# Kernel tuning notes

Measured on AMD Instinct MI355X. Metric: run time of the kernel, lower is better.

Reference implementation:

```python
import jax, jax.numpy as jnp
import numpy as np

B, M, IN, H, D = 64, 512, 256, 4, 64
N = B * M
E = N * 16


def setup_inputs() -> dict:
    key = jax.random.key(0)
    ks = jax.random.split(key, 12)
    s = 1.0 / np.sqrt(IN)
    return {
        "query_input": jax.random.normal(ks[0], (N, IN), jnp.float32),
        "source_input": jax.random.normal(ks[1], (N, IN), jnp.float32),
        "edge_weight": jax.random.uniform(ks[2], (E,), jnp.float32),
        "Wq_w": jax.random.normal(ks[3], (IN, H * D), jnp.float32) * s,
        "Wq_b": jax.random.normal(ks[4], (H * D,), jnp.float32) * s,
        "Wk_w": jax.random.normal(ks[5], (IN, H * D), jnp.float32) * s,
        "Wk_b": jax.random.normal(ks[6], (H * D,), jnp.float32) * s,
        "Wv_w": jax.random.normal(ks[7], (IN, H * D), jnp.float32) * s,
        "Wv_b": jax.random.normal(ks[8], (H * D,), jnp.float32) * s,
        "n_nodes": jnp.full((B,), M, jnp.int32),
        "edge_index": jax.random.randint(ks[9], (2, E), 0, N, jnp.int32),
    }


def reference(query_input, source_input, edge_weight, Wq_w, Wq_b, Wk_w, Wk_b, Wv_w, Wv_b, n_nodes, edge_index):
    # projections -> [N, H, D]
    q = (query_input @ Wq_w + Wq_b).reshape(N, H, D)
    k = (source_input @ Wk_w + Wk_b).reshape(N, H, D)
    v = (source_input @ Wv_w + Wv_b).reshape(N, H, D)

    # 'simple' kernel attention. Global L2 normalization (torch.norm over whole tensor).
    qn = q / jnp.linalg.norm(q)
    kn = k / jnp.linalg.norm(k)
    # equal-size graphs: padding + mask reduces exactly to a reshape [B, M, H, D]
    q_pad = qn.reshape(B, M, H, D)
    k_pad = kn.reshape(B, M, H, D)
    v_pad = v.reshape(B, M, H, D)
    kv = jnp.einsum('bmhk,bmhv->bhkv', k_pad, v_pad)          # per-graph K^T V
    v_sum = v_pad.sum(axis=1)                                  # [B, H, D] scatter_add over batch
    k_sum = k_pad.sum(axis=1)                                  # [B, H, D]
    numer = jnp.einsum('bmhk,bhkv->bmhv', q_pad, kv) + v_sum[:, None]
    denom = jnp.einsum('bmhk,bhk->bmh', q_pad, k_sum) + n_nodes.astype(q.dtype)[:, None, None]
    attn = (numer / denom[..., None]).reshape(N, H, D)

    # gcn_conv on value: out[c] = sum_{e: col_e = c} w_e * rsqrt(deg[col_e]*deg[row_e]) * v[row_e]
    row, col = edge_index[0], edge_index[1]
    deg = jax.ops.segment_sum(jnp.ones((E,), jnp.float32), col, num_segments=N)
    val = edge_weight / jnp.sqrt(deg[col] * deg[row])
    val = jnp.nan_to_num(val, nan=0.0, posinf=0.0, neginf=0.0)
    gcn = jax.ops.segment_sum(val[:, None, None] * v[row], col, num_segments=N)

    return (attn + gcn).mean(axis=1)  # mean over heads -> [N, D]
```

## Files before the change

### kernel.cpp

```cpp
#include <hip/hip_runtime.h>
#include <hip/hip_bf16.h>

#define NN 32768
#define BB 64
#define MM 512
#define HH 4
#define DD 64
#define INF 256
#define HD 256
#define EE 524288

typedef unsigned short ushort;
typedef unsigned int uint;
typedef short s16x8 __attribute__((ext_vector_type(8)));
typedef ushort u16x8 __attribute__((ext_vector_type(8)));
typedef float f32x4 __attribute__((ext_vector_type(4)));

__device__ __forceinline__ ushort f2bf(float f) {
    uint u = __float_as_uint(f);
    return (ushort)((u + 0x7fffu + ((u >> 16) & 1u)) >> 16);
}
__device__ __forceinline__ float bf2f(ushort u) {
    return __uint_as_float((uint)u << 16);
}
__device__ __forceinline__ uint pkbf(float x, float y) {
    __hip_bfloat162 h = __float22bfloat162_rn(make_float2(x, y));
    return *(uint*)&h;
}

#define GLD16(gp, lp) __builtin_amdgcn_global_load_lds( \
    (const __attribute__((address_space(1))) void*)(gp), \
    (__attribute__((address_space(3))) void*)(lp), 16, 0, 0)

__global__ __launch_bounds__(256) void prep_kernel(
    const float* __restrict__ Wq, const float* __restrict__ Wk,
    const float* __restrict__ Wv, ushort* __restrict__ WT,
    const int* __restrict__ ei, int* __restrict__ deg)
{
    const int bid = blockIdx.x;
    if (bid < 768) {
        const int id = bid * 256 + threadIdx.x;
        const int mat = id >> 16, rem = id & 65535;
        const int n = rem >> 8, kk = rem & 255;
        const float* W = (mat == 0) ? Wq : (mat == 1) ? Wk : Wv;
        WT[id] = f2bf(W[kk * 256 + n]);
    } else {
        const int e = (bid - 768) * 256 + threadIdx.x;
        atomicAdd(&deg[ei[EE + e]], 1);
    }
}

__global__ __launch_bounds__(256, 4) void qkv_scan(
    const float* __restrict__ Xq, const float* __restrict__ Xs,
    const ushort* __restrict__ WT,
    const float* __restrict__ bq, const float* __restrict__ bk,
    const float* __restrict__ bv,
    ushort* __restrict__ qo, ushort* __restrict__ ko, ushort* __restrict__ vo,
    float* __restrict__ sumsq,
    const int* __restrict__ deg, int* __restrict__ offsets)
{
    __shared__ ushort As[2][128 * 32];
    __shared__ ushort Bs[3][128 * 32];
    int*   part = (int*)&As[0][0];
    float* wred = (float*)&Bs[0][0];

    const int id = blockIdx.x;
    const int t = threadIdx.x;

    if (id == 0) {
        const int base = t * 128;
        int s = 0;
        for (int i = 0; i < 128; i += 4) {
            const int4 d = *(const int4*)&deg[base + i];
            s += d.x + d.y + d.z + d.w;
        }
        part[t] = s;
        __syncthreads();
        for (int off = 1; off < 256; off <<= 1) {
            int a = part[t];
            int b2 = (t >= off) ? part[t - off] : 0;
            __syncthreads();
            part[t] = a + b2;
            __syncthreads();
        }
        int run = (t == 0) ? 0 : part[t - 1];
        for (int i = 0; i < 128; i += 4) {
            const int4 d = *(const int4*)&deg[base + i];
            int4 o;
            o.x = run; run += d.x;
            o.y = run; run += d.y;
            o.z = run; run += d.z;
            o.w = run; run += d.w;
            *(int4*)&offsets[base + i] = o;
        }
        if (t == 255) offsets[NN] = run;
        return;
    }

    const int gid = id - 1;
    const int vv = (gid & 7) * 192 + (gid >> 3);
    const int rt = vv / 6, ct = vv % 6;
    const int wsel = ct >> 1;
    const float* A    = (wsel == 0) ? Xq : Xs;
    const ushort* W   = WT + (size_t)wsel * 65536;
    const float* bias = (wsel == 0) ? bq : (wsel == 1) ? bk : bv;
    ushort* C         = (wsel == 0) ? qo : (wsel == 1) ? ko : vo;
    const int row0 = rt * 128;
    const int col0 = (ct & 1) * 128;

    const int l = t & 63, w = t >> 6;
    const int fr = l & 15, q4 = l >> 4;
    const int wr = (w & 1) * 64, wc = (w >> 1) * 64;

    const int srow = (w << 4) + (l >> 2);
    const int scol = (l & 3) << 3;
    const float*  ga = &A[(size_t)(row0 + srow) * INF + scol];
    const ushort* gb = &W[(size_t)(col0 + srow) * INF + scol];
    const int lbase = (w << 9);

    f32x4 acc[4][4] = {};
    float4 aA0, aA1, aA2, aA3;
    float4 aB0, aB1, aB2, aB3;

#define QKV_ALOADA(k0) { \
    const float* p0 = ga + (k0); \
    const float* p1 = ga + (k0) + 64 * INF; \
    aA0 = *(const float4*)(p0);     aA1 = *(const float4*)(p0 + 4); \
    aA2 = *(const float4*)(p1);     aA3 = *(const float4*)(p1 + 4); }

#define QKV_ALOADB(k0) { \
    const float* p0 = ga + (k0); \
    const float* p1 = ga + (k0) + 64 * INF; \
    aB0 = *(const float4*)(p0);     aB1 = *(const float4*)(p0 + 4); \
    aB2 = *(const float4*)(p1);     aB3 = *(const float4*)(p1 + 4); }

#define QKV_AWRITEA(abuf) { \
    union { u16x8 v; uint u[4]; } c0, c1; \
    c0.u[0] = pkbf(aA0.x, aA0.y); c0.u[1] = pkbf(aA0.z, aA0.w); \
    c0.u[2] = pkbf(aA1.x, aA1.y); c0.u[3] = pkbf(aA1.z, aA1.w); \
    c1.u[0] = pkbf(aA2.x, aA2.y); c1.u[1] = pkbf(aA2.z, aA2.w); \
    c1.u[2] = pkbf(aA3.x, aA3.y); c1.u[3] = pkbf(aA3.z, aA3.w); \
    *(u16x8*)&As[abuf][srow * 32 + scol]        = c0.v; \
    *(u16x8*)&As[abuf][2048 + srow * 32 + scol] = c1.v; }

#define QKV_AWRITEB(abuf) { \
    union { u16x8 v; uint u[4]; } c0, c1; \
    c0.u[0] = pkbf(aB0.x, aB0.y); c0.u[1] = pkbf(aB0.z, aB0.w); \
    c0.u[2] = pkbf(aB1.x, aB1.y); c0.u[3] = pkbf(aB1.z, aB1.w); \
    c1.u[0] = pkbf(aB2.x, aB2.y); c1.u[1] = pkbf(aB2.z, aB2.w); \
    c1.u[2] = pkbf(aB3.x, aB3.y); c1.u[3] = pkbf(aB3.z, aB3.w); \
    *(u16x8*)&As[abuf][srow * 32 + scol]        = c0.v; \
    *(u16x8*)&As[abuf][2048 + srow * 32 + scol] = c1.v; }

#define QKV_BSTAGE(bbuf, k0) \
    GLD16(gb + (k0),            &Bs[bbuf][lbase]); \
    GLD16(gb + (k0) + 64 * INF, &Bs[bbuf][2048 + lbase]);

#define QKV_COMPUTE(abuf, bbuf) { \
    const int kg = q4 * 8; \
    s16x8 af[4], bfr[4]; \
    _Pragma("unroll") \
    for (int i = 0; i < 4; ++i) \
        af[i] = *(const s16x8*)&As[abuf][(wr + i * 16 + fr) * 32 + kg]; \
    _Pragma("unroll") \
    for (int j = 0; j < 4; ++j) \
        bfr[j] = *(const s16x8*)&Bs[bbuf][(wc + j * 16 + fr) * 32 + kg]; \
    _Pragma("unroll") \
    for (int i = 0; i < 4; ++i) \
    _Pragma("unroll") \
        for (int j = 0; j < 4; ++j) \
            acc[i][j] = __builtin_amdgcn_mfma_f32_16x16x32_bf16( \
                af[i], bfr[j], acc[i][j], 0, 0, 0); }

#define WAITN(n) asm volatile("s_waitcnt vmcnt(" #n ")" ::: "memory")
#define LGKM0   asm volatile("s_waitcnt lgkmcnt(0)" ::: "memory")
#define BAR     __builtin_amdgcn_s_barrier()

    QKV_ALOADA(0)
    QKV_BSTAGE(0, 0)
    QKV_ALOADB(32)
    QKV_BSTAGE(1, 32)

    WAITN(6); QKV_AWRITEA(0) LGKM0; BAR;
    QKV_ALOADA(64)  QKV_BSTAGE(2, 64)   QKV_COMPUTE(0, 0)
    WAITN(6); QKV_AWRITEB(1) LGKM0; BAR;
    QKV_ALOADB(96)  QKV_BSTAGE(0, 96)   QKV_COMPUTE(1, 1)
    WAITN(6); QKV_AWRITEA(0) LGKM0; BAR;
    QKV_ALOADA(128) QKV_BSTAGE(1, 128)  QKV_COMPUTE(0, 2)
    WAITN(6); QKV_AWRITEB(1) LGKM0; BAR;
    QKV_ALOADB(160) QKV_BSTAGE(2, 160)  QKV_COMPUTE(1, 0)
    WAITN(6); QKV_AWRITEA(0) LGKM0; BAR;
    QKV_ALOADA(192) QKV_BSTAGE(0, 192)  QKV_COMPUTE(0, 1)
    WAITN(6); QKV_AWRITEB(1) LGKM0; BAR;
    QKV_ALOADB(224) QKV_BSTAGE(1, 224)  QKV_COMPUTE(1, 2)
    WAITN(6); QKV_AWRITEA(0) LGKM0; BAR;
    QKV_COMPUTE(0, 0)
    WAITN(0); QKV_AWRITEB(1) LGKM0; BAR;
    QKV_COMPUTE(1, 1)

    float loc = 0.f;
#pragma unroll
    for (int j = 0; j < 4; ++j) {
        const int colg = col0 + wc + j * 16 + fr;
        const float bj = bias[colg];
#pragma unroll
        for (int i = 0; i < 4; ++i) {
            const int rowg = row0 + wr + i * 16 + q4 * 4;
            const float cv0 = acc[i][j][0] + bj;
            const float cv1 = acc[i][j][1] + bj;
            const float cv2 = acc[i][j][2] + bj;
            const float cv3 = acc[i][j][3] + bj;
            loc += cv0 * cv0 + cv1 * cv1 + cv2 * cv2 + cv3 * cv3;
            const uint p01 = pkbf(cv0, cv1);
            const uint p23 = pkbf(cv2, cv3);
            C[(size_t)(rowg + 0) * HD + colg] = (ushort)p01;
            C[(size_t)(rowg + 1) * HD + colg] = (ushort)(p01 >> 16);
            C[(size_t)(rowg + 2) * HD + colg] = (ushort)p23;
            C[(size_t)(rowg + 3) * HD + colg] = (ushort)(p23 >> 16);
        }
    }
    if (wsel < 2) {
#pragma unroll
        for (int off = 32; off > 0; off >>= 1) loc += __shfl_down(loc, off, 64);
        __syncthreads();
        if (l == 0) wred[w] = loc;
        __syncthreads();
        if (t == 0) atomicAdd(&sumsq[wsel], wred[0] + wred[1] + wred[2] + wred[3]);
    }
}

#define KVP 72
__global__ __launch_bounds__(256) void kv_vbar_bucket(
    const ushort* __restrict__ k16, const ushort* __restrict__ v16,
    ushort* __restrict__ kv16, float* __restrict__ ksum_f, float* __restrict__ vsum_f,
    float* __restrict__ vbar,
    const int* __restrict__ ei, const float* __restrict__ ew,
    const int* __restrict__ deg, const int* __restrict__ offsets,
    int* __restrict__ cursor, int2* __restrict__ pairbuf)
{
    __shared__ ushort kT[64 * KVP];
    __shared__ ushort vT[64 * KVP];
    const int bid = blockIdx.x;
    const int t = threadIdx.x;

    if (bid >= 1280) {
        const int e = (bid - 1280) * 256 + t;
        const int row = ei[e], col = ei[EE + e];
        const long long prod = (long long)deg[row] * (long long)deg[col];
        float val = 0.f;
        if (prod > 0) val = ew[e] * __frsqrt_rn((float)prod);
        const int pos = atomicAdd(&cursor[col], 1);
        pairbuf[offsets[col] + pos] = make_int2(row, __float_as_int(val));
        return;
    }
    if (bid >= 256) {
        const int idx = (bid - 256) * 256 + t;
        const int n = idx >> 3, d0 = (idx & 7) * 8;
        const ushort* vr = &v16[(size_t)n * HD + d0];
        u16x8 v0 = *(const u16x8*)(vr);
        u16x8 v1 = *(const u16x8*)(vr + 64);
        u16x8 v2 = *(const u16x8*)(vr + 128);
        u16x8 v3 = *(const u16x8*)(vr + 192);
        float o[8];
#pragma unroll
        for (int j = 0; j < 8; ++j)
            o[j] = 0.25f * (bf2f(v0[j]) + bf2f(v1[j]) + bf2f(v2[j]) + bf2f(v3[j]));
        float* vb = &vbar[(size_t)n * DD + d0];
        *(float4*)(vb)     = make_float4(o[0], o[1], o[2], o[3]);
        *(float4*)(vb + 4) = make_float4(o[4], o[5], o[6], o[7]);
        return;
    }

    const int h = bid & 3, b = bid >> 2;
    const int l = t & 63, w = t >> 6;
    const size_t base = (size_t)b * MM * HD + (size_t)h * DD;

    const int fr = l & 15, q4 = l >> 4, kg = q4 * 8;
    const int wr2 = (w & 1) * 32, wc2 = (w >> 1) * 32;
    s16x8 ones;
#pragma unroll
    for (int i = 0; i < 8; ++i) ones[i] = (short)0x3F80;

    f32x4 acc[2][2] = {};
    f32x4 aks[2] = {};
    f32x4 avs[2] = {};

    const int mat = t >> 7;
    const int rem = t & 127;
    const int dq  = rem >> 5;
    const int u   = rem & 31;
    const int r0  = 2 * u;
    const int d0  = dq * 16;
    const ushort* src = mat ? v16 : k16;
    ushort* dst = mat ? vT : kT;

    for (int chunk = 0; chunk < 8; ++chunk) {
        const int m0 = chunk * 64;
        {
            const ushort* p0 = &src[base + (size_t)(m0 + r0) * HD + d0];
            const ushort* p1 = p0 + HD;
            u16x8 ra0 = *(const u16x8*)(p0);
            u16x8 ra1 = *(const u16x8*)(p0 + 8);
            u16x8 rb0 = *(const u16x8*)(p1);
            u16x8 rb1 = *(const u16x8*)(p1 + 8);
#pragma unroll
            for (int jj = 0; jj < 8; ++jj) {
                uint pk = (uint)ra0[jj] | ((uint)rb0[jj] << 16);
                *(uint*)&dst[(d0 + jj) * KVP + r0] = pk;
            }
#pragma unroll
            for (int jj = 0; jj < 8; ++jj) {
                uint pk = (uint)ra1[jj] | ((uint)rb1[jj] << 16);
                *(uint*)&dst[(d0 + 8 + jj) * KVP + r0] = pk;
            }
        }
        __syncthreads();

#pragma unroll
        for (int s = 0; s < 2; ++s) {
            const int mo = s * 32 + kg;
            s16x8 af[2], bf[2];
            af[0] = *(const s16x8*)&kT[(wr2 + fr) * KVP + mo];
            af[1] = *(const s16x8*)&kT[(wr2 + 16 + fr) * KVP + mo];
            bf[0] = *(const s16x8*)&vT[(wc2 + fr) * KVP + mo];
            bf[1] = *(const s16x8*)&vT[(wc2 + 16 + fr) * KVP + mo];
#pragma unroll
            for (int il = 0; il < 2; ++il)
#pragma unroll
                for (int jl = 0; jl < 2; ++jl)
                    acc[il][jl] = __builtin_amdgcn_mfma_f32_16x16x32_bf16(
                        af[il], bf[jl], acc[il][jl], 0, 0, 0);
#pragma unroll
            for (int il = 0; il < 2; ++il)
                aks[il] = __builtin_amdgcn_mfma_f32_16x16x32_bf16(
                    af[il], ones, aks[il], 0, 0, 0);
#pragma unroll
            for (int jl = 0; jl < 2; ++jl)
                avs[jl] = __builtin_amdgcn_mfma_f32_16x16x32_bf16(
                    ones, bf[jl], avs[jl], 0, 0, 0);
        }
        __syncthreads();
    }

    ushort* kvb = &kv16[((size_t)b * HH + h) * 4096];
#pragma unroll
    for (int jl = 0; jl < 2; ++jl) {
        const int dv = wc2 + 16 * jl + fr;
#pragma unroll
        for (int il = 0; il < 2; ++il) {
            const int dk = wr2 + 16 * il + q4 * 4;
            uint2 pk = make_uint2(pkbf(acc[il][jl][0], acc[il][jl][1]),
                                  pkbf(acc[il][jl][2], acc[il][jl][3]));
            *(uint2*)&kvb[(size_t)dv * 64 + dk] = pk;
        }
    }
    float* ksb = &ksum_f[((size_t)b * HH + h) * 64];
    float* vsb = &vsum_f[((size_t)b * HH + h) * 64];
    if (wc2 == 0 && fr == 0) {
#pragma unroll
        for (int il = 0; il < 2; ++il)
#pragma unroll
            for (int m = 0; m < 4; ++m)
                ksb[wr2 + 16 * il + q4 * 4 + m] = aks[il][m];
    }
    if (wr2 == 0 && l < 16) {
        vsb[wc2 + l]      = avs[0][0];
        vsb[wc2 + 16 + l] = avs[1][0];
    }
}

#define AKP 72
__global__ __launch_bounds__(256) void attn_mfma(
    const ushort* __restrict__ q16, const ushort* __restrict__ kv16,
    const float* __restrict__ ksum_f, const float* __restrict__ vsum_f,
    const float* __restrict__ sumsq,
    const int* __restrict__ n_nodes, float* __restrict__ out)
{
    const int b = blockIdx.y;
    const int m0 = blockIdx.x * 64;
    const int t = threadIdx.x;
    const int l = t & 63, w = t >> 6;
    const int fr = l & 15, q4 = l >> 4;
    const int wn = (w & 1) * 32, wd = (w >> 1) * 32;

    __shared__ ushort kvbf[HH][64 * AKP];
    __shared__ float ksum_l[HH][64], vsum_l[HH][64], denom_l[HH][64];

    const float nn = (float)n_nodes[b];
    const float inv = 1.0f / (sqrtf(sumsq[0]) * sqrtf(sumsq[1]));

    {
        const int dv = t >> 2, dk0 = (t & 3) * 16;
#pragma unroll
        for (int h = 0; h < HH; ++h) {
            const ushort* kvg = &kv16[((size_t)(b * HH + h)) * 4096 + dv * 64 + dk0];
            *(uint4*)&kvbf[h][dv * AKP + dk0]     = *(const uint4*)kvg;
            *(uint4*)&kvbf[h][dv * AKP + dk0 + 8] = *(const uint4*)(kvg + 8);
        }
        const int hh = t >> 6, dd = t & 63;
        ksum_l[hh][dd] = ksum_f[((size_t)(b * HH + hh)) * 64 + dd];
        vsum_l[hh][dd] = vsum_f[((size_t)(b * HH + hh)) * 64 + dd];
    }
    __syncthreads();

    {
        const int r = t & 63, hh = t >> 6;
        const ushort* qr = &q16[((size_t)(b * MM + m0 + r)) * HD + hh * DD];
        float dsum = 0.f;
#pragma unroll
        for (int c = 0; c < 8; ++c) {
            u16x8 qv = *(const u16x8*)(qr + 8 * c);
#pragma unroll
            for (int j2 = 0; j2 < 8; ++j2)
                dsum += bf2f(qv[j2]) * ksum_l[hh][8 * c + j2];
        }
        denom_l[hh][r] = nn + inv * dsum;
    }
    __syncthreads();

    f32x4 acco[2][2] = {};
#pragma unroll
    for (int h = 0; h < HH; ++h) {
        f32x4 pacc[2][2] = {};
#pragma unroll
        for (int kx = 0; kx < 2; ++kx) {
            const int k0 = kx * 32;
            s16x8 af[2], bfr[2];
#pragma unroll
            for (int il = 0; il < 2; ++il)
                af[il] = *(const s16x8*)&q16[
                    ((size_t)(b * MM + m0 + wn + 16 * il + fr)) * HD + h * DD + k0 + q4 * 8];
#pragma unroll
            for (int jl = 0; jl < 2; ++jl)
                bfr[jl] = *(const s16x8*)&kvbf[h][(wd + 16 * jl + fr) * AKP + k0 + q4 * 8];
#pragma unroll
            for (int il = 0; il < 2; ++il)
#pragma unroll
                for (int jl = 0; jl < 2; ++jl)
                    pacc[il][jl] = __builtin_amdgcn_mfma_f32_16x16x32_bf16(
                        af[il], bfr[jl], pacc[il][jl], 0, 0, 0);
        }
#pragma unroll
        for (int il = 0; il < 2; ++il)
#pragma unroll
            for (int m = 0; m < 4; ++m) {
                const float rden = 0.25f / denom_l[h][wn + 16 * il + q4 * 4 + m];
#pragma unroll
                for (int jl = 0; jl < 2; ++jl) {
                    const int d = wd + 16 * jl + fr;
                    acco[il][jl][m] += (inv * pacc[il][jl][m] + vsum_l[h][d]) * rden;
                }
            }
    }

#pragma unroll
    for (int il = 0; il < 2; ++il)
#pragma unroll
        for (int m = 0; m < 4; ++m) {
            const size_t node = (size_t)b * MM + m0 + wn + 16 * il + q4 * 4 + m;
#pragma unroll
            for (int jl = 0; jl < 2; ++jl)
                out[node * DD + wd + 16 * jl + fr] = acco[il][jl][m];
        }
}

__global__ __launch_bounds__(256) void gcn_gather(
    const int* __restrict__ offsets, const int2* __restrict__ pairbuf,
    const float* __restrict__ vbar, float* __restrict__ out)
{
    const int t = blockIdx.x * 256 + threadIdx.x;
    const int n = t >> 5;
    const int g = t & 31;
    const int d4 = (g & 15) << 2;
    const int grp = g >> 4;
    const int s = offsets[n], e = offsets[n + 1];
    float ax = 0.f, ay = 0.f, az = 0.f, aw = 0.f;
    int i = s + grp;
    for (; i + 2 < e; i += 4) {
        const int2 p0 = pairbuf[i], p1 = pairbuf[i + 2];
        const float w0 = __int_as_float(p0.y), w1 = __int_as_float(p1.y);
        const float4 v0 = *(const float4*)&vbar[(size_t)p0.x * DD + d4];
        const float4 v1 = *(const float4*)&vbar[(size_t)p1.x * DD + d4];
        ax += w0 * v0.x + w1 * v1.x;
        ay += w0 * v0.y + w1 * v1.y;
        az += w0 * v0.z + w1 * v1.z;
        aw += w0 * v0.w + w1 * v1.w;
    }
    if (i < e) {
        const int2 p = pairbuf[i];
        const float wv = __int_as_float(p.y);
        const float4 v = *(const float4*)&vbar[(size_t)p.x * DD + d4];
        ax += wv * v.x; ay += wv * v.y; az += wv * v.z; aw += wv * v.w;
    }
    ax += __shfl_xor(ax, 16, 64);
    ay += __shfl_xor(ay, 16, 64);
    az += __shfl_xor(az, 16, 64);
    aw += __shfl_xor(aw, 16, 64);
    if (grp == 0) {
        float4 o = *(float4*)&out[(size_t)n * DD + d4];
        o.x += ax; o.y += ay; o.z += az; o.w += aw;
        *(float4*)&out[(size_t)n * DD + d4] = o;
    }
}

extern "C" void kernel_launch(void* const* d_in, const int* in_sizes, int n_in,
                              void* d_out, int out_size, void* d_ws, size_t ws_size,
                              hipStream_t stream)
{
    (void)in_sizes; (void)n_in; (void)out_size; (void)ws_size;
    const float* Xq = (const float*)d_in[0];
    const float* Xs = (const float*)d_in[1];
    const float* ew = (const float*)d_in[2];
    const float* Wq = (const float*)d_in[3];
    const float* bq = (const float*)d_in[4];
    const float* Wk = (const float*)d_in[5];
    const float* bk = (const float*)d_in[6];
    const float* Wv = (const float*)d_in[7];
    const float* bv = (const float*)d_in[8];
    const int* n_nodes = (const int*)d_in[9];
    const int* ei = (const int*)d_in[10];
    float* out = (float*)d_out;
    float* ws  = (float*)d_ws;

    const size_t SZ_QKV   = (size_t)NN * HD / 2;
    const size_t OFF_Q    = 0;
    const size_t OFF_K    = SZ_QKV;
    const size_t OFF_V    = SZ_QKV * 2;
    const size_t OFF_SS   = SZ_QKV * 3;
    const size_t OFF_DEG  = OFF_SS + 16;
    const size_t OFF_CUR  = OFF_DEG + NN;
    const size_t OFF_WT   = OFF_CUR + NN;
    const size_t OFF_OFFS = OFF_WT + 3 * 65536 / 2;
    const size_t OFF_KV16 = OFF_OFFS + NN + 16;
    const size_t OFF_KSF  = OFF_KV16 + (size_t)BB * HH * 4096 / 2;
    const size_t OFF_VSF  = OFF_KSF + (size_t)BB * HH * 64;
    const size_t OFF_PAIR = OFF_VSF + (size_t)BB * HH * 64;
    const size_t OFF_VBAR = OFF_PAIR + 2 * (size_t)EE;

    ushort* q16   = (ushort*)(ws + OFF_Q);
    ushort* k16   = (ushort*)(ws + OFF_K);
    ushort* v16   = (ushort*)(ws + OFF_V);
    float* sumsq  = ws + OFF_SS;
    int*   deg    = (int*)(ws + OFF_DEG);
    int*   cursor = (int*)(ws + OFF_CUR);
    ushort* WT    = (ushort*)(ws + OFF_WT);
    int*   offs   = (int*)(ws + OFF_OFFS);
    ushort* kv16  = (ushort*)(ws + OFF_KV16);
    float* ksum_f = ws + OFF_KSF;
    float* vsum_f = ws + OFF_VSF;
    int2*  pairb  = (int2*)(ws + OFF_PAIR);
    float* vbar   = ws + OFF_VBAR;

    hipMemsetAsync(sumsq, 0, (16 + 2 * NN) * sizeof(float), stream);
    prep_kernel<<<2816, 256, 0, stream>>>(Wq, Wk, Wv, WT, ei, deg);
    qkv_scan<<<1537, 256, 0, stream>>>(
        Xq, Xs, WT, bq, bk, bv, q16, k16, v16, sumsq, deg, offs);
    kv_vbar_bucket<<<3328, 256, 0, stream>>>(
        k16, v16, kv16, ksum_f, vsum_f, vbar, ei, ew, deg, offs, cursor, pairb);
    attn_mfma<<<dim3(MM / 64, BB), 256, 0, stream>>>(
        q16, kv16, ksum_f, vsum_f, sumsq, n_nodes, out);
    gcn_gather<<<(NN * 32) / 256, 256, 0, stream>>>(offs, pairb, vbar, out);
}
```

Baseline: 239.5 us.

## Fuse GCN neighbor gather into attention kernel epilogue

New measurement: 240.5 us. No clear change (+0.4%).

```diff
diff --git a/kernel.cpp b/kernel.cpp
--- a/kernel.cpp
+++ b/kernel.cpp
@@ -370,11 +370,13 @@
 }
 
 #define AKP 72
-__global__ __launch_bounds__(256) void attn_mfma(
+__global__ __launch_bounds__(256) void attn_gcn(
     const ushort* __restrict__ q16, const ushort* __restrict__ kv16,
     const float* __restrict__ ksum_f, const float* __restrict__ vsum_f,
     const float* __restrict__ sumsq,
-    const int* __restrict__ n_nodes, float* __restrict__ out)
+    const int* __restrict__ n_nodes,
+    const int* __restrict__ offsets, const int2* __restrict__ pairbuf,
+    const float* __restrict__ vbar, float* __restrict__ out)
 {
     const int b = blockIdx.y;
     const int m0 = blockIdx.x * 64;
@@ -385,6 +387,7 @@
 
     __shared__ ushort kvbf[HH][64 * AKP];
     __shared__ float ksum_l[HH][64], vsum_l[HH][64], denom_l[HH][64];
+    float* gcn_l = (float*)&kvbf[0][0];
 
     const float nn = (float)n_nodes[b];
     const float inv = 1.0f / (sqrtf(sumsq[0]) * sqrtf(sumsq[1]));
@@ -452,55 +455,54 @@
                 }
             }
     }
+    __syncthreads();
+
+    {
+        const int r = t >> 2, qq = t & 3;
+        const int d16 = qq * 16;
+        const int node = b * MM + m0 + r;
+        const int s = offsets[node], e = offsets[node + 1];
+        f32x4 g0 = {}, g1 = {}, g2 = {}, g3 = {};
+        int i = s;
+        for (; i + 1 < e; i += 2) {
+            const int2 p0 = pairbuf[i], p1 = pairbuf[i + 1];
+            const float v0 = __int_as_float(p0.y), v1 = __int_as_float(p1.y);
+            const float* r0 = &vbar[(size_t)p0.x * DD + d16];
+            const float* r1 = &vbar[(size_t)p1.x * DD + d16];
+            g0 += v0 * *(const f32x4*)(r0)      + v1 * *(const f32x4*)(r1);
+            g1 += v0 * *(const f32x4*)(r0 + 4)  + v1 * *(const f32x4*)(r1 + 4);
+            g2 += v0 * *(const f32x4*)(r0 + 8)  + v1 * *(const f32x4*)(r1 + 8);
+            g3 += v0 * *(const f32x4*)(r0 + 12) + v1 * *(const f32x4*)(r1 + 12);
+        }
+        if (i < e) {
+            const int2 p = pairbuf[i];
+            const float v = __int_as_float(p.y);
+            const float* rr = &vbar[(size_t)p.x * DD + d16];
+            g0 += v * *(const f32x4*)(rr);
+            g1 += v * *(const f32x4*)(rr + 4);
+            g2 += v * *(const f32x4*)(rr + 8);
+            g3 += v * *(const f32x4*)(rr + 12);
+        }
+        float* gl = &gcn_l[r * 64 + d16];
+        *(f32x4*)(gl)      = g0;
+        *(f32x4*)(gl + 4)  = g1;
+        *(f32x4*)(gl + 8)  = g2;
+        *(f32x4*)(gl + 12) = g3;
+    }
+    __syncthreads();
 
 #pragma unroll
     for (int il = 0; il < 2; ++il)
 #pragma unroll
         for (int m = 0; m < 4; ++m) {
-            const size_t node = (size_t)b * MM + m0 + wn + 16 * il + q4 * 4 + m;
-#pragma unroll
-            for (int jl = 0; jl < 2; ++jl)
-                out[node * DD + wd + 16 * jl + fr] = acco[il][jl][m];
-        }
-}
-
-__global__ __launch_bounds__(256) void gcn_gather(
-    const int* __restrict__ offsets, const int2* __restrict__ pairbuf,
-    const float* __restrict__ vbar, float* __restrict__ out)
-{
-    const int t = blockIdx.x * 256 + threadIdx.x;
-    const int n = t >> 5;
-    const int g = t & 31;
-    const int d4 = (g & 15) << 2;
-    const int grp = g >> 4;
-    const int s = offsets[n], e = offsets[n + 1];
-    float ax = 0.f, ay = 0.f, az = 0.f, aw = 0.f;
-    int i = s + grp;
-    for (; i + 2 < e; i += 4) {
-        const int2 p0 = pairbuf[i], p1 = pairbuf[i + 2];
-        const float w0 = __int_as_float(p0.y), w1 = __int_as_float(p1.y);
-        const float4 v0 = *(const float4*)&vbar[(size_t)p0.x * DD + d4];
-        const float4 v1 = *(const float4*)&vbar[(size_t)p1.x * DD + d4];
-        ax += w0 * v0.x + w1 * v1.x;
-        ay += w0 * v0.y + w1 * v1.y;
-        az += w0 * v0.z + w1 * v1.z;
-        aw += w0 * v0.w + w1 * v1.w;
-    }
-    if (i < e) {
-        const int2 p = pairbuf[i];
-        const float wv = __int_as_float(p.y);
-        const float4 v = *(const float4*)&vbar[(size_t)p.x * DD + d4];
-        ax += wv * v.x; ay += wv * v.y; az += wv * v.z; aw += wv * v.w;
-    }
-    ax += __shfl_xor(ax, 16, 64);
-    ay += __shfl_xor(ay, 16, 64);
-    az += __shfl_xor(az, 16, 64);
-    aw += __shfl_xor(aw, 16, 64);
-    if (grp == 0) {
-        float4 o = *(float4*)&out[(size_t)n * DD + d4];
-        o.x += ax; o.y += ay; o.z += az; o.w += aw;
-        *(float4*)&out[(size_t)n * DD + d4] = o;
-    }
+            const int rl = wn + 16 * il + q4 * 4 + m;
+            const size_t node = (size_t)b * MM + m0 + rl;
+#pragma unroll
+            for (int jl = 0; jl < 2; ++jl) {
+                const int d = wd + 16 * jl + fr;
+                out[node * DD + d] = acco[il][jl][m] + gcn_l[rl * 64 + d];
+            }
+        }
 }
 
 extern "C" void kernel_launch(void* const* d_in, const int* in_sizes, int n_in,
@@ -557,7 +559,6 @@
         Xq, Xs, WT, bq, bk, bv, q16, k16, v16, sumsq, deg, offs);
     kv_vbar_bucket<<<3328, 256, 0, stream>>>(
         k16, v16, kv16, ksum_f, vsum_f, vbar, ei, ew, deg, offs, cursor, pairb);
-    attn_mfma<<<dim3(MM / 64, BB), 256, 0, stream>>>(
-        q16, kv16, ksum_f, vsum_f, sumsq, n_nodes, out);
-    gcn_gather<<<(NN * 32) / 256, 256, 0, stream>>>(offs, pairb, vbar, out);
-}
+    attn_gcn<<<dim3(MM / 64, BB), 256, 0, stream>>>(
+        q16, kv16, ksum_f, vsum_f, sumsq, n_nodes, offs, pairb, vbar, out);
+}
```
